# Kernel optimization log

Measured on AMD Instinct MI355X. Metric: run time of the kernel, lower is better.

The kernel has to match this reference:

```python
import jax, jax.numpy as jnp
import numpy as np

D_MODEL = 1024
N_HEAD = 16
N_BR = 4
DH = D_MODEL // N_HEAD            # 64
H_TOT = N_BR * N_HEAD             # 64
SCALE = float(np.pi / np.sqrt(3.0))
ATTN_SCALE = DH ** -0.5


def _rope(x):
    # x: (B, H, T, Dh). Non-interleaved variant: output is cat of the two rotated halves.
    B, H, T, Dh = x.shape
    inv_freq = 1.0 / (10000.0 ** (jnp.arange(0, Dh, 2, dtype=jnp.float32) / Dh))  # (Dh/2,)
    t = jnp.arange(T, dtype=jnp.float32)
    freqs = t[:, None] * inv_freq[None, :]        # (T, Dh/2)
    cos = jnp.cos(freqs)[None, None]              # (1,1,T,Dh/2)
    sin = jnp.sin(freqs)[None, None]
    x1 = x[..., 0::2]
    x2 = x[..., 1::2]
    return jnp.concatenate([-x2 * sin + x1 * cos, x1 * sin + x2 * cos], axis=-1)


def setup_inputs() -> dict:
    key = jax.random.key(0)
    ks = jax.random.split(key, 8)
    s = 0.02
    B, T = 1, 1024
    return {
        "X": jax.random.normal(ks[0], (B, T, D_MODEL), jnp.float32),
        "Wq": jax.random.normal(ks[1], (D_MODEL, H_TOT * DH), jnp.float32) * s,
        "bq": jnp.zeros((H_TOT * DH,), jnp.float32),
        "Wk": jax.random.normal(ks[2], (D_MODEL, D_MODEL), jnp.float32) * s,
        "bk": jnp.zeros((D_MODEL,), jnp.float32),
        "Wv": jax.random.normal(ks[3], (D_MODEL, H_TOT * DH), jnp.float32) * s,
        "bv": jnp.zeros((H_TOT * DH,), jnp.float32),
        "sink_scalars": jax.random.normal(ks[4], (H_TOT, 1, 1), jnp.float32) * s,
        "v_nulls": jax.random.normal(ks[5], (H_TOT, DH), jnp.float32) * s,
        "Wo": jax.random.normal(ks[6], (D_MODEL, D_MODEL), jnp.float32) * s,
        "bo": jnp.zeros((D_MODEL,), jnp.float32),
    }


def reference(X, Wq, bq, Wk, bk, Wv, bv, sink_scalars, v_nulls, Wo, bo):
    B, T, C = X.shape
    q = (X @ Wq + bq).reshape(B, T, H_TOT, DH).transpose(0, 2, 1, 3)   # (B,H,T,Dh)
    v = (X @ Wv + bv).reshape(B, T, H_TOT, DH).transpose(0, 2, 1, 3)
    k_base = (X @ Wk + bk).reshape(B, T, N_HEAD, DH).transpose(0, 2, 1, 3)  # (B,Nh,T,Dh)
    k = jnp.tile(k_base, (1, N_BR, 1, 1))                               # (B,H,T,Dh)

    q = _rope(q)
    k = _rope(k)

    scores = jnp.einsum('bhtd,bhsd->bhts', q, k) * ATTN_SCALE           # (B,H,T,T)
    key_self = jnp.clip(jnp.sum(k * k, axis=-1), 1e-6, None)            # (B,H,T)
    denom = jnp.sqrt(key_self)[:, :, None, :]                           # (B,H,1,T)
    w = jax.nn.softplus(scores / denom)

    causal = jnp.tril(jnp.ones((T, T), dtype=bool))                     # keep lower triangle
    w = jnp.where(causal[None, None], w, 0.0)
    w = w * jax.nn.sigmoid(SCALE * w)

    sinks = jnp.tanh(sink_scalars).reshape(1, H_TOT, 1, 1) + 1e-6       # (1,H,1,1)
    alpha = 1.0 / (jnp.sum(w, axis=-1, keepdims=True) + sinks + 1e-6)   # (B,H,T,1)
    probs_tokens = w * alpha
    probs_sink = sinks * alpha                                          # (B,H,T,1)

    out_tokens = jnp.einsum('bhts,bhsd->bhtd', probs_tokens, v)
    out_sinks = probs_sink * v_nulls[None, :, None, :]                  # (B,H,T,Dh)
    context = out_tokens + out_sinks                                    # (B,H,T,Dh)

    context = context.reshape(B, N_BR, N_HEAD, T, DH)
    context = context.transpose(0, 1, 3, 2, 4).reshape(B, N_BR, T, C)
    y = context @ Wo + bo                                               # (B,N_BR,T,C)
    return jnp.mean(y, axis=1)


if __name__ == "__main__":
    out = reference(**setup_inputs())
    print(out.shape)
```

## Files before the change

kernel.cpp:

```cpp
#include <hip/hip_runtime.h>
#include <math.h>

#define SILU_SCALE 1.8137993642342178f
#define QKV_N 9216
#define LN2 0.6931471805599453f
#define DNSCALE 0.18033688011112042f

typedef __attribute__((ext_vector_type(8))) short bf16x8;
typedef __attribute__((ext_vector_type(4))) float f32x4;

#if __has_builtin(__builtin_amdgcn_exp2f)
#define EXP2(x) __builtin_amdgcn_exp2f(x)
#else
#define EXP2(x) exp2f(x)
#endif
#if __has_builtin(__builtin_amdgcn_logf)
#define LOG2(x) __builtin_amdgcn_logf(x)
#else
#define LOG2(x) __log2f(x)
#endif

__device__ __forceinline__ unsigned short f2bf(float f){
    union { float f; unsigned int i; } u; u.f = f;
    unsigned int r = u.i + 0x7FFFu + ((u.i >> 16) & 1u);
    return (unsigned short)(r >> 16);
}
__device__ __forceinline__ float bf2f(unsigned short s){
    union { unsigned int i; float f; } u; u.i = ((unsigned int)s) << 16;
    return u.f;
}
__device__ __forceinline__ unsigned int pack_bf2(float lo, float hi){
    unsigned int i0 = __float_as_uint(lo) + 0x8000u;
    unsigned int i1 = __float_as_uint(hi) + 0x8000u;
    return __builtin_amdgcn_perm(i1, i0, 0x07060302u);
}

__device__ __forceinline__ void gload_lds16(const void* g, void* l){
    __builtin_amdgcn_global_load_lds(
        (const __attribute__((address_space(1))) void*)g,
        (__attribute__((address_space(3))) void*)l, 16, 0, 0);
}

__global__ __launch_bounds__(256) void prep_kernel(
    const float* __restrict__ X,
    const float* __restrict__ Wq, const float* __restrict__ Wk,
    const float* __restrict__ Wv, const float* __restrict__ Wo,
    const float* __restrict__ bq, const float* __restrict__ bk,
    const float* __restrict__ bv,
    unsigned short* __restrict__ Xb, unsigned short* __restrict__ WqkvT,
    unsigned short* __restrict__ WoT, float* __restrict__ qkvb)
{
    __shared__ float t[64][65];
    int b = blockIdx.x;
    const int tid = threadIdx.x;

    if (b >= 2560){
        if (b < 3072){
            int i = ((b - 2560) * 256 + tid) * 8;
            float4 a = *(const float4*)&X[i];
            float4 c = *(const float4*)&X[i + 4];
            union { unsigned short u[8]; uint4 v; } o;
            o.u[0]=f2bf(a.x); o.u[1]=f2bf(a.y); o.u[2]=f2bf(a.z); o.u[3]=f2bf(a.w);
            o.u[4]=f2bf(c.x); o.u[5]=f2bf(c.y); o.u[6]=f2bf(c.z); o.u[7]=f2bf(c.w);
            *(uint4*)&Xb[i] = o.v;
        } else {
            int i = (b - 3072) * 256 + tid;
            float v;
            if (i < 4096) v = bq[i];
            else if (i < 5120) v = bk[i - 4096];
            else v = bv[i - 5120];
            qkvb[i] = v;
        }
        return;
    }

    const float* W; unsigned short* Wt; int N, tiles_x;
    if (b < 1024)      { W = Wq; Wt = WqkvT;                       N = 4096; tiles_x = 64; }
    else if (b < 1280) { b -= 1024; W = Wk; Wt = WqkvT + (size_t)4096*1024; N = 1024; tiles_x = 16; }
    else if (b < 2304) { b -= 1280; W = Wv; Wt = WqkvT + (size_t)5120*1024; N = 4096; tiles_x = 64; }
    else               { b -= 2304; W = Wo; Wt = WoT;              N = 1024; tiles_x = 16; }

    const int k0 = (b / tiles_x) * 64, n0 = (b % tiles_x) * 64;
    const int lr  = tid >> 4;
    const int lc4 = (tid & 15) * 4;
    #pragma unroll
    for (int p = 0; p < 4; p++){
        int r = lr + p * 16;
        float4 v = *(const float4*)&W[(size_t)(k0 + r) * N + n0 + lc4];
        t[lc4+0][r] = v.x; t[lc4+1][r] = v.y;
        t[lc4+2][r] = v.z; t[lc4+3][r] = v.w;
    }
    __syncthreads();
    const int wr  = tid >> 3;
    const int wc8 = (tid & 7) * 8;
    #pragma unroll
    for (int p = 0; p < 2; p++){
        int r = wr + p * 32;
        union { unsigned short u[8]; uint4 v; } o;
        #pragma unroll
        for (int j = 0; j < 8; j++) o.u[j] = f2bf(t[r][wc8 + j]);
        *(uint4*)&Wt[(size_t)(n0 + r) * 1024 + k0 + wc8] = o.v;
    }
}

template<int BM, int BN, int OUTBF>
__global__ __launch_bounds__(256) void gemm_k(
    const unsigned short* __restrict__ A,
    const unsigned short* __restrict__ Bt,
    const float* __restrict__ bias,
    void* __restrict__ Cout, int M, int N, int K)
{
    constexpr int MT = BM / 32;
    constexpr int NT = BN / 32;
    __shared__ unsigned short As[BM * 64];
    __shared__ unsigned short Bs[BN * 64];
    const int tid  = threadIdx.x;
    const int wave = tid >> 6;
    const int lane = tid & 63;
    const int l15  = lane & 15;
    const int quad = lane >> 4;
    const int m0 = blockIdx.y * BM;
    const int n0 = blockIdx.x * BN;
    const int wm = (wave >> 1) * (BM / 2);
    const int wn = (wave & 1) * (BN / 2);

    f32x4 acc[MT][NT];
    #pragma unroll
    for (int i = 0; i < MT; i++)
        #pragma unroll
        for (int j = 0; j < NT; j++)
            acc[i][j] = (f32x4){0.f, 0.f, 0.f, 0.f};

    for (int k0 = 0; k0 < K; k0 += 64){
        #pragma unroll
        for (int j = 0; j < (BM * 8) / 256; j++){
            int bslot = j * 256 + wave * 64;
            int slot = bslot + lane;
            int row = slot >> 3, phys = slot & 7;
            int c = phys ^ (row & 7);
            gload_lds16(&A[(size_t)(m0 + row) * K + k0 + c * 8], &As[bslot * 8]);
        }
        #pragma unroll
        for (int j = 0; j < (BN * 8) / 256; j++){
            int bslot = j * 256 + wave * 64;
            int slot = bslot + lane;
            int row = slot >> 3, phys = slot & 7;
            int c = phys ^ (row & 7);
            gload_lds16(&Bt[(size_t)(n0 + row) * K + k0 + c * 8], &Bs[bslot * 8]);
        }
        __syncthreads();
        #pragma unroll
        for (int ks = 0; ks < 2; ks++){
            bf16x8 af[MT], bfr[NT];
            #pragma unroll
            for (int i = 0; i < MT; i++){
                int row = wm + i * 16 + l15;
                int phys = (ks * 4 + quad) ^ (row & 7);
                af[i] = *(const bf16x8*)&As[row * 64 + phys * 8];
            }
            #pragma unroll
            for (int j = 0; j < NT; j++){
                int row = wn + j * 16 + l15;
                int phys = (ks * 4 + quad) ^ (row & 7);
                bfr[j] = *(const bf16x8*)&Bs[row * 64 + phys * 8];
            }
            #pragma unroll
            for (int i = 0; i < MT; i++)
                #pragma unroll
                for (int j = 0; j < NT; j++)
                    acc[i][j] = __builtin_amdgcn_mfma_f32_16x16x32_bf16(af[i], bfr[j], acc[i][j], 0, 0, 0);
        }
        __syncthreads();
    }
    #pragma unroll
    for (int i = 0; i < MT; i++){
        #pragma unroll
        for (int j = 0; j < NT; j++){
            int col = n0 + wn + j * 16 + l15;
            float bv = bias[col];
            #pragma unroll
            for (int r = 0; r < 4; r++){
                int row = m0 + wm + i * 16 + quad * 4 + r;
                float v = acc[i][j][r] + bv;
                if (OUTBF) ((unsigned short*)Cout)[(size_t)row * N + col] = f2bf(v);
                else       ((float*)Cout)[(size_t)row * N + col] = v;
            }
        }
    }
}

__global__ __launch_bounds__(256) void gemm_wo(
    const unsigned short* __restrict__ A,
    const unsigned short* __restrict__ Bt,
    float* __restrict__ P)
{
    constexpr int BM = 128, BN = 64, MT = 4, NT = 2;
    __shared__ unsigned short As[BM * 64];
    __shared__ unsigned short Bs[BN * 64];
    const int tid  = threadIdx.x;
    const int wave = tid >> 6;
    const int lane = tid & 63;
    const int l15  = lane & 15;
    const int quad = lane >> 4;
    const int m0 = blockIdx.y * BM;
    const int n0 = blockIdx.x * BN;
    const int kz = blockIdx.z;
    const int wm = (wave >> 1) * 64;
    const int wn = (wave & 1) * 32;

    f32x4 acc[MT][NT];
    #pragma unroll
    for (int i = 0; i < MT; i++)
        #pragma unroll
        for (int j = 0; j < NT; j++)
            acc[i][j] = (f32x4){0.f, 0.f, 0.f, 0.f};

    const int kbeg = kz * 512;
    for (int k0 = kbeg; k0 < kbeg + 512; k0 += 64){
        #pragma unroll
        for (int j = 0; j < (BM * 8) / 256; j++){
            int bslot = j * 256 + wave * 64;
            int slot = bslot + lane;
            int row = slot >> 3, phys = slot & 7;
            int c = phys ^ (row & 7);
            gload_lds16(&A[(size_t)(m0 + row) * 1024 + k0 + c * 8], &As[bslot * 8]);
        }
        #pragma unroll
        for (int j = 0; j < (BN * 8) / 256; j++){
            int bslot = j * 256 + wave * 64;
            int slot = bslot + lane;
            int row = slot >> 3, phys = slot & 7;
            int c = phys ^ (row & 7);
            gload_lds16(&Bt[(size_t)(n0 + row) * 1024 + k0 + c * 8], &Bs[bslot * 8]);
        }
        __syncthreads();
        #pragma unroll
        for (int ks = 0; ks < 2; ks++){
            bf16x8 af[MT], bfr[NT];
            #pragma unroll
            for (int i = 0; i < MT; i++){
                int row = wm + i * 16 + l15;
                int phys = (ks * 4 + quad) ^ (row & 7);
                af[i] = *(const bf16x8*)&As[row * 64 + phys * 8];
            }
            #pragma unroll
            for (int j = 0; j < NT; j++){
                int row = wn + j * 16 + l15;
                int phys = (ks * 4 + quad) ^ (row & 7);
                bfr[j] = *(const bf16x8*)&Bs[row * 64 + phys * 8];
            }
            #pragma unroll
            for (int i = 0; i < MT; i++)
                #pragma unroll
                for (int j = 0; j < NT; j++)
                    acc[i][j] = __builtin_amdgcn_mfma_f32_16x16x32_bf16(af[i], bfr[j], acc[i][j], 0, 0, 0);
        }
        __syncthreads();
    }
    float* Pz = P + (size_t)kz * 1024 * 1024;
    #pragma unroll
    for (int i = 0; i < MT; i++){
        #pragma unroll
        for (int j = 0; j < NT; j++){
            int col = n0 + wn + j * 16 + l15;
            #pragma unroll
            for (int r = 0; r < 4; r++){
                int row = m0 + wm + i * 16 + quad * 4 + r;
                Pz[(size_t)row * 1024 + col] = acc[i][j][r];
            }
        }
    }
}

__global__ void wo_reduce(const float* __restrict__ P, const float* __restrict__ bo,
                          float* __restrict__ out)
{
    int i = (blockIdx.x * 256 + threadIdx.x) * 4;
    float4 a = *(const float4*)&P[i];
    float4 b = *(const float4*)&P[1024 * 1024 + i];
    float4 c = *(const float4*)&bo[i & 1023];
    float4 o;
    o.x = a.x + b.x + c.x; o.y = a.y + b.y + c.y;
    o.z = a.z + b.z + c.z; o.w = a.w + b.w + c.w;
    *(float4*)&out[i] = o;
}

__global__ void rope_k(unsigned short* __restrict__ qkv, float* __restrict__ dninv)
{
    int idx = blockIdx.x * blockDim.x + threadIdx.x;
    int t = idx >> 4, h = idx & 15;
    unsigned short* p = qkv + (size_t)t * QKV_N + 4096 + h * 64;
    uint4 raw[8];
    #pragma unroll
    for (int i = 0; i < 8; i++) raw[i] = *(const uint4*)(p + i * 8);
    const unsigned short* rp = (const unsigned short*)raw;
    float x[64];
    #pragma unroll
    for (int i = 0; i < 64; i++) x[i] = bf2f(rp[i]);
    unsigned short o[64];
    float ss = 0.f;
    #pragma unroll
    for (int d = 0; d < 32; d++){
        float inv = EXP2(-(float)d * 0.4152410118609203f);
        float s, c; __sincosf((float)t * inv, &s, &c);
        float x1 = x[2*d], x2 = x[2*d+1];
        float a = x1 * c - x2 * s;
        float b = x1 * s + x2 * c;
        ss = fmaf(a, a, fmaf(b, b, ss));
        o[d]      = f2bf(a);
        o[d + 32] = f2bf(b);
    }
    #pragma unroll
    for (int i = 0; i < 8; i++) *(uint4*)(p + i * 8) = ((const uint4*)o)[i];
    dninv[h * 1024 + t] = DNSCALE * rsqrtf(fmaxf(ss, 1e-6f));
}

__global__ __launch_bounds__(256) void attn_mfma(
    const unsigned short* __restrict__ qkv,
    const float* __restrict__ dninv,
    const float* __restrict__ sinks, const float* __restrict__ vnulls,
    unsigned short* __restrict__ ctx)
{
    __shared__ unsigned short ks[64 * 64];
    __shared__ unsigned short vt[64 * 64];
    __shared__ unsigned short ws[64][72];
    __shared__ float dl[64];
    __shared__ float dsum[4][16];

    const int tid  = threadIdx.x;
    const int wave = tid >> 6;
    const int lane = tid & 63;
    const int l15  = lane & 15;
    const int quad = lane >> 4;
    const int h  = blockIdx.x;
    const int kh = h & 15;
    const int qt = 15 - blockIdx.y;
    const int t0 = qt << 6;

    const unsigned short* Q  = qkv;
    const unsigned short* Kp = qkv + 4096;
    const unsigned short* V  = qkv + 5120;

    bf16x8 qf0, qf1;
    {
        const int t = t0 + wave * 16 + l15;
        const unsigned short* qp = Q + (size_t)t * QKV_N + h * 64 + quad * 16;
        uint4 r0 = *(const uint4*)qp;
        uint4 r1 = *(const uint4*)(qp + 8);
        unsigned short e[16];
        *(uint4*)&e[0] = r0; *(uint4*)&e[8] = r1;
        unsigned short o0[8], o1[8];
        #pragma unroll
        for (int j = 0; j < 8; j++){
            int dp = quad * 8 + j;
            float inv = EXP2(-(float)dp * 0.4152410118609203f);
            float s, c; __sincosf((float)t * inv, &s, &c);
            float x1 = bf2f(e[2*j]), x2 = bf2f(e[2*j+1]);
            o0[j] = f2bf(x1 * c - x2 * s);
            o1[j] = f2bf(x1 * s + x2 * c);
        }
        qf0 = *(const bf16x8*)o0;
        qf1 = *(const bf16x8*)o1;
    }

    f32x4 acc_o[4];
    #pragma unroll
    for (int i = 0; i < 4; i++) acc_o[i] = (f32x4){0.f, 0.f, 0.f, 0.f};
    float den = 0.f;
    const int q_glob = t0 + wave * 16 + l15;

    const int pr  = tid >> 3;
    const int cch = tid & 7;

    for (int st = 0; st <= qt; st++){
        const int s0 = st << 6;
        __syncthreads();

        #pragma unroll
        for (int i = 0; i < 2; i++){
            int bslot = wave * 128 + i * 64;
            int slot = bslot + lane;
            int row = slot >> 3, phys = slot & 7;
            int c = phys ^ (row & 7);
            gload_lds16(&Kp[(size_t)(s0 + row) * QKV_N + kh * 64 + c * 8], &ks[bslot * 8]);
        }
        {
            uint4 g0 = *(const uint4*)&V[(size_t)(s0 + 2 * pr)     * QKV_N + h * 64 + cch * 8];
            uint4 g1 = *(const uint4*)&V[(size_t)(s0 + 2 * pr + 1) * QKV_N + h * 64 + cch * 8];
            const unsigned short* p0 = (const unsigned short*)&g0;
            const unsigned short* p1 = (const unsigned short*)&g1;
            #pragma unroll
            for (int j = 0; j < 8; j++){
                int d = cch * 8 + j;
                int physc = (pr >> 2) ^ ((d ^ (d >> 3)) & 7);
                unsigned int val = (unsigned int)p0[j] | ((unsigned int)p1[j] << 16);
                ((unsigned int*)vt)[d * 32 + physc * 4 + (pr & 3)] = val;
            }
        }
        if (tid < 64) dl[tid] = dninv[kh * 1024 + s0 + tid];
        __syncthreads();

        const bool diag = (st == qt);

        #pragma unroll
        for (int nt = 0; nt < 4; nt++){
            const int sbase = nt * 16 + quad * 4;
            uint2* wp = (uint2*)&ws[wave * 16 + l15][sbase];
            if (diag && nt > wave){ *wp = (uint2){0u, 0u}; continue; }

            f32x4 sc = (f32x4){0.f, 0.f, 0.f, 0.f};
            {
                int srow = nt * 16 + l15;
                int ph0 = quad ^ (srow & 7);
                int ph1 = (4 + quad) ^ (srow & 7);
                bf16x8 kf0 = *(const bf16x8*)&ks[srow * 64 + ph0 * 8];
                bf16x8 kf1 = *(const bf16x8*)&ks[srow * 64 + ph1 * 8];
                sc = __builtin_amdgcn_mfma_f32_16x16x32_bf16(kf0, qf0, sc, 0, 0, 0);
                sc = __builtin_amdgcn_mfma_f32_16x16x32_bf16(kf1, qf1, sc, 0, 0, 0);
            }
            float da[4];
            *(float4*)da = *(const float4*)&dl[sbase];
            float w4[4];
            #pragma unroll
            for (int r = 0; r < 4; r++){
                float y = sc[r] * da[r];
                float p = EXP2(-fabsf(y));
                float u = fmaxf(y, 0.f) + LOG2(1.f + p);
                float e3 = EXP2(-SILU_SCALE * u);
                float wv = __fdividef(LN2 * u, 1.f + e3);
                wv = (s0 + sbase + r <= q_glob) ? wv : 0.f;
                den += wv;
                w4[r] = wv;
            }
            uint2 pk;
            pk.x = pack_bf2(w4[0], w4[1]);
            pk.y = pack_bf2(w4[2], w4[3]);
            *wp = pk;
        }

        {
            const int prow = wave * 16 + l15;
            bf16x8 pf0 = *(const bf16x8*)&ws[prow][quad * 8];
            bf16x8 pf1 = *(const bf16x8*)&ws[prow][32 + quad * 8];
            const bool skip_hi = diag && (wave <= 1);
            #pragma unroll
            for (int dt = 0; dt < 4; dt++){
                int d = dt * 16 + l15;
                int swz = (d ^ (d >> 3)) & 7;
                bf16x8 vf0 = *(const bf16x8*)&vt[d * 64 + (quad ^ swz) * 8];
                acc_o[dt] = __builtin_amdgcn_mfma_f32_16x16x32_bf16(pf0, vf0, acc_o[dt], 0, 0, 0);
                if (!skip_hi){
                    bf16x8 vf1 = *(const bf16x8*)&vt[d * 64 + ((4 + quad) ^ swz) * 8];
                    acc_o[dt] = __builtin_amdgcn_mfma_f32_16x16x32_bf16(pf1, vf1, acc_o[dt], 0, 0, 0);
                }
            }
        }
    }

    den += __shfl_xor(den, 16);
    den += __shfl_xor(den, 32);
    if (quad == 0) dsum[wave][l15] = den;
    float den4[4];
    *(float4*)den4 = *(const float4*)&dsum[wave][quad * 4];

    float sinkv = tanhf(sinks[h]) + 1e-6f;
    #pragma unroll
    for (int r = 0; r < 4; r++){
        int qg = t0 + wave * 16 + quad * 4 + r;
        float alpha = __fdividef(1.f, den4[r] + sinkv + 1e-6f);
        #pragma unroll
        for (int dt = 0; dt < 4; dt++){
            int d = dt * 16 + l15;
            float o = (acc_o[dt][r] + sinkv * vnulls[h * 64 + d]) * alpha;
            ctx[((size_t)h * 1024 + qg) * 64 + d] = f2bf(o);
        }
    }
}

__global__ void avg_kernel(const unsigned short* __restrict__ ctx, unsigned short* __restrict__ avg)
{
    int i8 = (blockIdx.x * 256 + threadIdx.x) * 8;
    int t = i8 >> 10, c = i8 & 1023;
    int nh = c >> 6, d = c & 63;
    float s[8] = {};
    #pragma unroll
    for (int br = 0; br < 4; br++){
        uint4 v = *(const uint4*)&ctx[((size_t)(br * 16 + nh) * 1024 + t) * 64 + d];
        const unsigned short* p = (const unsigned short*)&v;
        #pragma unroll
        for (int j = 0; j < 8; j++) s[j] += bf2f(p[j]);
    }
    union { unsigned short u[8]; uint4 v; } o;
    #pragma unroll
    for (int j = 0; j < 8; j++) o.u[j] = f2bf(0.25f * s[j]);
    *(uint4*)&avg[i8] = o.v;
}

extern "C" void kernel_launch(void* const* d_in, const int* in_sizes, int n_in,
                              void* d_out, int out_size, void* d_ws, size_t ws_size,
                              hipStream_t stream)
{
    (void)in_sizes; (void)n_in; (void)out_size; (void)ws_size;
    const float* X      = (const float*)d_in[0];
    const float* Wq     = (const float*)d_in[1];
    const float* bq     = (const float*)d_in[2];
    const float* Wk     = (const float*)d_in[3];
    const float* bk     = (const float*)d_in[4];
    const float* Wv     = (const float*)d_in[5];
    const float* bv     = (const float*)d_in[6];
    const float* sinks  = (const float*)d_in[7];
    const float* vnulls = (const float*)d_in[8];
    const float* Wo     = (const float*)d_in[9];
    const float* bo     = (const float*)d_in[10];
    float* out = (float*)d_out;

    unsigned short* w16   = (unsigned short*)d_ws;
    unsigned short* Xb    = w16;
    unsigned short* WqkvT = Xb    + (size_t)1024 * 1024;
    unsigned short* QKVb  = WqkvT + (size_t)QKV_N * 1024;
    unsigned short* WoT   = QKVb  + (size_t)1024 * QKV_N;
    unsigned short* ctxb  = WoT   + (size_t)1024 * 1024;
    unsigned short* avgb  = ctxb  + (size_t)64 * 1024 * 64;
    float* qkvb = (float*)(avgb + (size_t)1024 * 1024);
    float* dnf  = qkvb + QKV_N;
    float* pWo  = (float*)WqkvT;

    dim3 blk(256);
    prep_kernel<<<3108, blk, 0, stream>>>(X, Wq, Wk, Wv, Wo, bq, bk, bv,
                                          Xb, WqkvT, WoT, qkvb);
    gemm_k<128, 96, 1><<<dim3(96, 8), blk, 0, stream>>>(Xb, WqkvT, qkvb, QKVb, 1024, QKV_N, 1024);
    rope_k<<<64, blk, 0, stream>>>(QKVb, dnf);
    attn_mfma<<<dim3(64, 16), blk, 0, stream>>>(QKVb, dnf, sinks, vnulls, ctxb);
    avg_kernel<<<512, blk, 0, stream>>>(ctxb, avgb);
    gemm_wo<<<dim3(16, 8, 2), blk, 0, stream>>>(avgb, WoT, pWo);
    wo_reduce<<<1024, blk, 0, stream>>>(pWo, bo, out);
}
```

Measured before the change: 201.4 us.

## Pre-transpose V in postproc kernel and register-prefetch K/V tiles in attention

The rope kernel becomes a combined postproc kernel that also writes a transposed copy of V per head into workspace that the QKV weights no longer need. The attention loop then loads K and pre-transposed V tiles into registers one iteration ahead and stores them to LDS with plain vector stores. This replaces the async global-to-LDS K load and the per-element V transpose scatter inside the loop. It costs an extra global write and read of V and more registers per thread, and the workspace layout is reshuffled to fit the new buffer.

```diff
diff --git a/kernel.cpp b/kernel.cpp
--- a/kernel.cpp
+++ b/kernel.cpp
@@ -285,38 +285,71 @@
     *(float4*)&out[i] = o;
 }
 
-__global__ void rope_k(unsigned short* __restrict__ qkv, float* __restrict__ dninv)
-{
-    int idx = blockIdx.x * blockDim.x + threadIdx.x;
-    int t = idx >> 4, h = idx & 15;
-    unsigned short* p = qkv + (size_t)t * QKV_N + 4096 + h * 64;
-    uint4 raw[8];
-    #pragma unroll
-    for (int i = 0; i < 8; i++) raw[i] = *(const uint4*)(p + i * 8);
-    const unsigned short* rp = (const unsigned short*)raw;
-    float x[64];
-    #pragma unroll
-    for (int i = 0; i < 64; i++) x[i] = bf2f(rp[i]);
-    unsigned short o[64];
-    float ss = 0.f;
-    #pragma unroll
-    for (int d = 0; d < 32; d++){
-        float inv = EXP2(-(float)d * 0.4152410118609203f);
-        float s, c; __sincosf((float)t * inv, &s, &c);
-        float x1 = x[2*d], x2 = x[2*d+1];
-        float a = x1 * c - x2 * s;
-        float b = x1 * s + x2 * c;
-        ss = fmaf(a, a, fmaf(b, b, ss));
-        o[d]      = f2bf(a);
-        o[d + 32] = f2bf(b);
-    }
-    #pragma unroll
-    for (int i = 0; i < 8; i++) *(uint4*)(p + i * 8) = ((const uint4*)o)[i];
-    dninv[h * 1024 + t] = DNSCALE * rsqrtf(fmaxf(ss, 1e-6f));
+__global__ __launch_bounds__(256) void postproc_kernel(
+    unsigned short* __restrict__ qkv, float* __restrict__ dninv,
+    unsigned short* __restrict__ VT)
+{
+    int b = blockIdx.x;
+    const int tid = threadIdx.x;
+    if (b < 64){
+        int idx = b * 256 + tid;
+        int t = idx >> 4, h = idx & 15;
+        unsigned short* p = qkv + (size_t)t * QKV_N + 4096 + h * 64;
+        uint4 raw[8];
+        #pragma unroll
+        for (int i = 0; i < 8; i++) raw[i] = *(const uint4*)(p + i * 8);
+        const unsigned short* rp = (const unsigned short*)raw;
+        float x[64];
+        #pragma unroll
+        for (int i = 0; i < 64; i++) x[i] = bf2f(rp[i]);
+        unsigned short o[64];
+        float ss = 0.f;
+        #pragma unroll
+        for (int d = 0; d < 32; d++){
+            float inv = EXP2(-(float)d * 0.4152410118609203f);
+            float s, c; __sincosf((float)t * inv, &s, &c);
+            float x1 = x[2*d], x2 = x[2*d+1];
+            float a = x1 * c - x2 * s;
+            float bb = x1 * s + x2 * c;
+            ss = fmaf(a, a, fmaf(bb, bb, ss));
+            o[d]      = f2bf(a);
+            o[d + 32] = f2bf(bb);
+        }
+        #pragma unroll
+        for (int i = 0; i < 8; i++) *(uint4*)(p + i * 8) = ((const uint4*)o)[i];
+        dninv[h * 1024 + t] = DNSCALE * rsqrtf(fmaxf(ss, 1e-6f));
+        return;
+    }
+    b -= 64;
+    const int h = b >> 4, s0 = (b & 15) * 64;
+    __shared__ unsigned short tile[64 * 64];
+    const unsigned short* V = qkv + 5120;
+    const int pr = tid >> 3, cch = tid & 7;
+    uint4 g0 = *(const uint4*)&V[(size_t)(s0 + 2 * pr)     * QKV_N + h * 64 + cch * 8];
+    uint4 g1 = *(const uint4*)&V[(size_t)(s0 + 2 * pr + 1) * QKV_N + h * 64 + cch * 8];
+    const unsigned short* p0 = (const unsigned short*)&g0;
+    const unsigned short* p1 = (const unsigned short*)&g1;
+    #pragma unroll
+    for (int j = 0; j < 8; j++){
+        int d = cch * 8 + j;
+        int physc = (pr >> 2) ^ ((d ^ (d >> 3)) & 7);
+        unsigned int val = (unsigned int)p0[j] | ((unsigned int)p1[j] << 16);
+        ((unsigned int*)tile)[d * 32 + physc * 4 + (pr & 3)] = val;
+    }
+    __syncthreads();
+    #pragma unroll
+    for (int i = 0; i < 2; i++){
+        int slot = tid + i * 256;
+        int d = slot >> 3, c = slot & 7;
+        int phys = c ^ ((d ^ (d >> 3)) & 7);
+        uint4 v = *(const uint4*)&tile[d * 64 + phys * 8];
+        *(uint4*)&VT[((size_t)h * 64 + d) * 1024 + s0 + c * 8] = v;
+    }
 }
 
 __global__ __launch_bounds__(256) void attn_mfma(
     const unsigned short* __restrict__ qkv,
+    const unsigned short* __restrict__ VT,
     const float* __restrict__ dninv,
     const float* __restrict__ sinks, const float* __restrict__ vnulls,
     unsigned short* __restrict__ ctx)
@@ -339,7 +372,12 @@
 
     const unsigned short* Q  = qkv;
     const unsigned short* Kp = qkv + 4096;
-    const unsigned short* V  = qkv + 5120;
+    const unsigned short* Vh = VT + (size_t)h * 64 * 1024;
+
+    const int srow0 = tid >> 3,        sphy0 = tid & 7;
+    const int srow1 = (tid + 256) >> 3, sphy1 = tid & 7;
+    const int sc0 = sphy0 ^ (srow0 & 7);
+    const int sc1 = sphy1 ^ (srow1 & 7);
 
     bf16x8 qf0, qf1;
     {
@@ -369,35 +407,34 @@
     float den = 0.f;
     const int q_glob = t0 + wave * 16 + l15;
 
-    const int pr  = tid >> 3;
-    const int cch = tid & 7;
+    uint4 kr0, kr1, vr0, vr1;
+    float dreg = 0.f;
+    {
+        kr0 = *(const uint4*)&Kp[(size_t)srow0 * QKV_N + kh * 64 + sc0 * 8];
+        kr1 = *(const uint4*)&Kp[(size_t)srow1 * QKV_N + kh * 64 + sc1 * 8];
+        vr0 = *(const uint4*)&Vh[(size_t)srow0 * 1024 + sc0 * 8];
+        vr1 = *(const uint4*)&Vh[(size_t)srow1 * 1024 + sc1 * 8];
+        if (tid < 64) dreg = dninv[kh * 1024 + tid];
+    }
 
     for (int st = 0; st <= qt; st++){
         const int s0 = st << 6;
         __syncthreads();
 
-        #pragma unroll
-        for (int i = 0; i < 2; i++){
-            int bslot = wave * 128 + i * 64;
-            int slot = bslot + lane;
-            int row = slot >> 3, phys = slot & 7;
-            int c = phys ^ (row & 7);
-            gload_lds16(&Kp[(size_t)(s0 + row) * QKV_N + kh * 64 + c * 8], &ks[bslot * 8]);
-        }
-        {
-            uint4 g0 = *(const uint4*)&V[(size_t)(s0 + 2 * pr)     * QKV_N + h * 64 + cch * 8];
-            uint4 g1 = *(const uint4*)&V[(size_t)(s0 + 2 * pr + 1) * QKV_N + h * 64 + cch * 8];
-            const unsigned short* p0 = (const unsigned short*)&g0;
-            const unsigned short* p1 = (const unsigned short*)&g1;
-            #pragma unroll
-            for (int j = 0; j < 8; j++){
-                int d = cch * 8 + j;
-                int physc = (pr >> 2) ^ ((d ^ (d >> 3)) & 7);
-                unsigned int val = (unsigned int)p0[j] | ((unsigned int)p1[j] << 16);
-                ((unsigned int*)vt)[d * 32 + physc * 4 + (pr & 3)] = val;
-            }
-        }
-        if (tid < 64) dl[tid] = dninv[kh * 1024 + s0 + tid];
+        *(uint4*)&ks[(size_t)tid * 8]         = kr0;
+        *(uint4*)&ks[(size_t)(tid + 256) * 8] = kr1;
+        *(uint4*)&vt[(size_t)tid * 8]         = vr0;
+        *(uint4*)&vt[(size_t)(tid + 256) * 8] = vr1;
+        if (tid < 64) dl[tid] = dreg;
+
+        if (st < qt){
+            const int sn = (st + 1) << 6;
+            kr0 = *(const uint4*)&Kp[(size_t)(sn + srow0) * QKV_N + kh * 64 + sc0 * 8];
+            kr1 = *(const uint4*)&Kp[(size_t)(sn + srow1) * QKV_N + kh * 64 + sc1 * 8];
+            vr0 = *(const uint4*)&Vh[(size_t)srow0 * 1024 + sn + sc0 * 8];
+            vr1 = *(const uint4*)&Vh[(size_t)srow1 * 1024 + sn + sc1 * 8];
+            if (tid < 64) dreg = dninv[kh * 1024 + sn + tid];
+        }
         __syncthreads();
 
         const bool diag = (st == qt);
@@ -446,11 +483,11 @@
             #pragma unroll
             for (int dt = 0; dt < 4; dt++){
                 int d = dt * 16 + l15;
-                int swz = (d ^ (d >> 3)) & 7;
-                bf16x8 vf0 = *(const bf16x8*)&vt[d * 64 + (quad ^ swz) * 8];
+                int sw = d & 7;
+                bf16x8 vf0 = *(const bf16x8*)&vt[d * 64 + (quad ^ sw) * 8];
                 acc_o[dt] = __builtin_amdgcn_mfma_f32_16x16x32_bf16(pf0, vf0, acc_o[dt], 0, 0, 0);
                 if (!skip_hi){
-                    bf16x8 vf1 = *(const bf16x8*)&vt[d * 64 + ((4 + quad) ^ swz) * 8];
+                    bf16x8 vf1 = *(const bf16x8*)&vt[d * 64 + ((4 + quad) ^ sw) * 8];
                     acc_o[dt] = __builtin_amdgcn_mfma_f32_16x16x32_bf16(pf1, vf1, acc_o[dt], 0, 0, 0);
                 }
             }
@@ -523,14 +560,15 @@
     unsigned short* avgb  = ctxb  + (size_t)64 * 1024 * 64;
     float* qkvb = (float*)(avgb + (size_t)1024 * 1024);
     float* dnf  = qkvb + QKV_N;
-    float* pWo  = (float*)WqkvT;
+    unsigned short* VTb = WqkvT;
+    float* pWo = (float*)(WqkvT + (size_t)4 * 1024 * 1024);
 
     dim3 blk(256);
     prep_kernel<<<3108, blk, 0, stream>>>(X, Wq, Wk, Wv, Wo, bq, bk, bv,
                                           Xb, WqkvT, WoT, qkvb);
     gemm_k<128, 96, 1><<<dim3(96, 8), blk, 0, stream>>>(Xb, WqkvT, qkvb, QKVb, 1024, QKV_N, 1024);
-    rope_k<<<64, blk, 0, stream>>>(QKVb, dnf);
-    attn_mfma<<<dim3(64, 16), blk, 0, stream>>>(QKVb, dnf, sinks, vnulls, ctxb);
+    postproc_kernel<<<1088, blk, 0, stream>>>(QKVb, dnf, VTb);
+    attn_mfma<<<dim3(64, 16), blk, 0, stream>>>(QKVb, VTb, dnf, sinks, vnulls, ctxb);
     avg_kernel<<<512, blk, 0, stream>>>(ctxb, avgb);
     gemm_wo<<<dim3(16, 8, 2), blk, 0, stream>>>(avgb, WoT, pWo);
     wo_reduce<<<1024, blk, 0, stream>>>(pWo, bo, out);
```

New measurement: 192.4 us. 1.05x faster.
